# Kernel tuning notes

Measured on AMD Instinct MI355X. Metric: run time of the kernel, lower is better.

## Reference

```python
import jax, jax.numpy as jnp
import numpy as np
import math

C64 = jnp.complex64

def _fftconv_full(a, kern):
    # full linear convolution along last axis (complex), like scipy.signal.fftconvolve
    L = a.shape[-1] + kern.shape[0] - 1
    A = jnp.fft.fft(a, n=L, axis=-1)
    K = jnp.fft.fft(kern.astype(a.dtype), n=L)
    return jnp.fft.ifft(A * K, axis=-1)

def _centered_ifft(f):
    # out[shft] = ifft(f[shft]) * sqrt(N), shft = (arange(N)+fix(N/2)) % N
    N = f.shape[-1]
    shft = (np.arange(N) + int(np.fix(N / 2))) % N
    inv = np.argsort(shft)
    g = jnp.fft.ifft(f[..., shft], axis=-1) * math.sqrt(N)
    return g[..., inv].astype(f.dtype)

def _sincinterp(f):
    # zero-stuff by 2 then sinc-filter; returns length 2N-1 along last axis
    N = f.shape[-1]
    y = jnp.zeros(f.shape[:-1] + (2 * N - 1,), f.dtype).at[..., ::2].set(f)
    kern = jnp.asarray(np.sinc(np.arange(-(2 * N - 3), 2 * N - 2) / 2.0).astype(np.complex64))
    return _fftconv_full(y, kern)[..., 2 * N - 3: 4 * N - 4]

def _frft_chirp(f, a):
    # Ozaktas chirp-convolution discrete FrFT, valid for 0.5 <= a <= 1.5
    N = f.shape[-1]
    alpha = a * math.pi / 2
    tana2, sina = math.tan(alpha / 2), math.sin(alpha)
    fi = _sincinterp(f)                                   # [..., 2N-1]
    pad = jnp.zeros(f.shape[:-1] + (N - 1,), f.dtype)
    fp = jnp.concatenate([pad, fi, pad], axis=-1)         # [..., 4N-3]
    n = np.arange(-2 * N + 2, 2 * N - 1).astype(np.float64)
    chrp = jnp.asarray(np.exp(-1j * math.pi / N * tana2 / 4 * n ** 2).astype(np.complex64))
    fp = chrp * fp
    c = math.pi / N / sina / 4
    m = np.arange(-(4 * N - 4), 4 * N - 3).astype(np.float64)
    kern = jnp.asarray(np.exp(1j * c * m ** 2).astype(np.complex64))
    ret = _fftconv_full(fp, kern)[..., 4 * N - 4: 8 * N - 7] * math.sqrt(c / math.pi)
    ret = chrp * ret
    phase = np.complex64(np.exp(-1j * (1 - a) * math.pi / 4))
    return phase * ret[..., N - 1: 3 * N - 2: 2]          # [..., N]

def _frft_last(f, a):
    # torch branch logic for the a values used here: a=0.5 (fwd), a=-0.5 (inv)
    if a < 0.5:
        f = _centered_ifft(f)
        a = a + 1.0
    return _frft_chirp(f, a)

def _frft2d(x, a):
    t = _frft_last(x, a)                                  # rows: along W
    return jnp.swapaxes(_frft_last(jnp.swapaxes(t, -1, -2), a), -1, -2)  # cols: along H

def _c1x1(x, w, b=None):
    y = jnp.einsum('nchw,oc->nohw', x, w)
    return y if b is None else y + b[None, :, None, None]

def _c3x3(x, w, b):
    y = jax.lax.conv_general_dilated(x, w, (1, 1), 'SAME',
                                     dimension_numbers=('NCHW', 'OIHW', 'NCHW'))
    return y + b[None, :, None, None]

def _forward(x, conv1_w, mag_s_w, mag_s_b, mag_f_w, mag_f_b, mag_w, mag_b,
             pha_w, pha_b, conv_0_w, conv_0_b, conv_1_w, conv_1_b, conv2_w):
    angle = 0.5
    alpha = math.cos(angle * math.pi / 2)
    N, C, H, W = x.shape
    H1, W1 = int(H * alpha), int(W * alpha)
    x1 = _c1x1(x, conv1_w)                                # stride=1 -> downsample is identity
    C1, C0 = C // 4, C // 4 // 3
    x_0, x_05, x_1 = x1[:, :C0], x1[:, C0:C1 - C0], x1[:, C1 - C0:C1]
    h0, w0 = (H - H1) // 2, (W - W1) // 2
    mask1 = jnp.zeros((H, W), jnp.float32).at[h0:h0 + H1, w0:w0 + W1].set(1.0)
    mask2 = 1.0 - mask1
    # fractional Fourier branch
    Fre = _frft2d(x_05.astype(C64), angle)
    mag, pha = jnp.abs(Fre), jnp.angle(Fre)
    mag_out = _c1x1(_c3x3(mag * mask1, mag_s_w, mag_s_b) * mask1
                    + _c1x1(mag * mask2, mag_f_w, mag_f_b) * mask2, mag_w, mag_b)
    pha_out = _c1x1(pha, pha_w, pha_b)
    Fre_out = jax.lax.complex(mag_out * jnp.cos(pha_out), mag_out * jnp.sin(pha_out))
    ifrft = jnp.abs(_frft2d(Fre_out, -angle))
    # plain Fourier branch (conv_1 applied to both mag and pha, as in the source)
    fre = jnp.fft.rfft2(x_1)
    fm, fp = jnp.abs(fre), jnp.angle(fre)
    mo = _c1x1(fm, conv_1_w, conv_1_b)
    po = _c1x1(fp, conv_1_w, conv_1_b)
    x_1o = jnp.fft.irfft2(jax.lax.complex(mo * jnp.cos(po), mo * jnp.sin(po)), s=(H, W))
    x_0o = _c1x1(x_0, conv_0_w, conv_0_b)
    return _c1x1(jnp.concatenate([x_0o, ifrft, x_1o], axis=1), conv2_w)

def setup_inputs():
    key = jax.random.key(0)
    ks = jax.random.split(key, 16)
    N, C, H, W, Co = 4, 192, 128, 128, 192
    C1, C0 = C // 4, C // 4 // 3
    Cm = C1 - 2 * C0
    s = 0.05
    r = lambda k, sh: jax.random.normal(k, sh, jnp.float32)
    return {
        "x": r(ks[0], (N, C, H, W)),
        "conv1_w": r(ks[1], (C1, C)) * s,
        "mag_s_w": r(ks[2], (Cm, Cm, 3, 3)) * s, "mag_s_b": r(ks[3], (Cm,)) * s,
        "mag_f_w": r(ks[4], (Cm, Cm)) * s, "mag_f_b": r(ks[5], (Cm,)) * s,
        "mag_w": r(ks[6], (Cm, Cm)) * s, "mag_b": r(ks[7], (Cm,)) * s,
        "pha_w": r(ks[8], (Cm, Cm)) * s, "pha_b": r(ks[9], (Cm,)) * s,
        "conv_0_w": r(ks[10], (C0, C0)) * s, "conv_0_b": r(ks[11], (C0,)) * s,
        "conv_1_w": r(ks[12], (C0, C0)) * s, "conv_1_b": r(ks[13], (C0,)) * s,
        "conv2_w": r(ks[14], (Co, C1)) * s,
    }

def reference(x, conv1_w, mag_s_w, mag_s_b, mag_f_w, mag_f_b, mag_w, mag_b,
              pha_w, pha_b, conv_0_w, conv_0_b, conv_1_w, conv_1_b, conv2_w):
    return _forward(x, conv1_w, mag_s_w, mag_s_b, mag_f_w, mag_f_b, mag_w, mag_b,
                    pha_w, pha_b, conv_0_w, conv_0_b, conv_1_w, conv_1_b, conv2_w)
```

## Files before the change

### kernel.cpp

```cpp
#include <hip/hip_runtime.h>
#include <math.h>

#define PI_D 3.14159265358979323846
#define TWO_PI_F 6.2831853071795864f

__device__ __align__(16) float2 g_Mf [128*128];
__device__ __align__(16) float2 g_MfT[128*128];
__device__ __align__(16) float2 g_Mb [128*128];
__device__ __align__(16) float2 g_MbT[128*128];
__device__ __align__(16) float2 g_F  [128*128];
__device__ __align__(16) float2 g_IF [128*128];
__device__ __align__(16) float  g_x1 [4*48*16384];
__device__ __align__(16) float2 g_bufA[64*16384];
__device__ __align__(16) float2 g_bufB[64*16384];
__device__ __align__(16) float  g_mag[64*16384];
__device__ __align__(16) float  g_pha[64*16384];
__device__ __align__(16) float  g_m65[64*8320];
__device__ __align__(16) float  g_p65[64*8320];
__device__ __align__(16) float  g_t1 [64*16384];
__device__ __align__(16) float  g_t2 [64*16384];
__device__ __align__(16) float  g_t3 [64*8320];
__device__ __align__(16) float  g_t4 [64*8320];
__device__ __align__(16) float  g_cat[4*48*16384];

__device__ inline void build_A_body(int tid) {
    if (tid >= 128*128) return;
    int o = tid >> 7, m = tid & 127;
    const double chc = -PI_D/128.0 * tan(PI_D/8.0) * 0.25;
    const double c   =  PI_D/(512.0*sin(PI_D/4.0));
    const double inv2pi = 1.0/(2.0*PI_D);
    float sr, si;
    {
        int n1 = 2*m - 127, tt = 2*(o - m);
        double ang = chc*(double)(n1*n1) + c*(double)(tt*tt);
        double r = ang*inv2pi; r -= floor(r);
        float af = (float)(r*2.0*PI_D);
        float sn, cs; __sincosf(af, &sn, &cs);
        sr = cs; si = sn;
    }
    for (int j = 0; j < 127; ++j) {
        int q  = 2*j + 1;
        int n1 = q - 127, tt = 2*o - q, d = q - 2*m;
        double ang = chc*(double)(n1*n1) + c*(double)(tt*tt);
        double r = ang*inv2pi; r -= floor(r);
        float af = (float)(r*2.0*PI_D);
        float s = (((d-1)>>1) & 1) ? -2.0f : 2.0f;
        s /= (3.14159265358979f*(float)d);
        float sn, cs; __sincosf(af, &sn, &cs);
        sr += s*cs; si += s*sn;
    }
    int n2 = 2*o - 127;
    double ph = chc*(double)(n2*n2) - PI_D/8.0;
    double r = ph*inv2pi; r -= floor(r);
    float pf = (float)(r*2.0*PI_D);
    float scale = (float)sqrt(c/PI_D);
    float sn, cs; __sincosf(pf, &sn, &cs);
    float cr = cs*scale, ci = sn*scale;
    float2 v = make_float2(sr*cr - si*ci, sr*ci + si*cr);
    g_Mf[tid] = v;
    g_MfT[(m<<7) + o] = v;
    int p = (o*m) & 127;
    float ang2 = TWO_PI_F*(float)p/128.0f;
    float sn2, cs2; __sincosf(ang2, &sn2, &cs2);
    g_F[tid]  = make_float2(cs2, -sn2);
    g_IF[tid] = make_float2(cs2*0.0078125f, sn2*0.0078125f);
}

template<int LM>
__device__ inline void load_T4(float2* tr, const float* mp, const float* pp,
                               const float* Trl, int hh, int w4) {
    if (LM == 1) {
        float4 v = *(const float4*)(Trl + (hh<<7) + w4);
        tr[0] = make_float2(v.x, 0.f); tr[1] = make_float2(v.y, 0.f);
        tr[2] = make_float2(v.z, 0.f); tr[3] = make_float2(v.w, 0.f);
    } else if (LM == 2) {
#pragma unroll
        for (int i = 0; i < 4; ++i) {
            int idx = (hh<<7) + w4 + i;
            float m = mp[idx], ph = pp[idx];
            float sn, cs; __sincosf(ph, &sn, &cs);
            tr[i] = make_float2(m*cs, m*sn);
        }
    } else {
#pragma unroll
        for (int i = 0; i < 4; ++i) {
            int w = w4 + i;
            int h2 = hh, w2 = w; float sg = 1.f;
            if (w >= 65) { h2 = (128 - hh) & 127; w2 = 128 - w; sg = -1.f; }
            int idx = h2*65 + w2;
            float m = mp[idx], ph = pp[idx];
            float sn, cs; __sincosf(ph, &sn, &cs);
            tr[i] = make_float2(m*cs, sg*m*sn);
        }
    }
}

__device__ inline void cfma(float2& a, float sx, float sy, float mx, float my) {
    a.x = fmaf(sx, mx, a.x); a.x = fmaf(-sy, my, a.x);
    a.y = fmaf(sx, my, a.y); a.y = fmaf(sy, mx, a.y);
}

template<int LM>
__device__ inline void rmul_body(const float2* __restrict__ MT, const float* __restrict__ Trl,
                                 const float* __restrict__ mp_, const float* __restrict__ pp_,
                                 float2* __restrict__ out, int cstart,
                                 int p, int r0, int t, float2* Ssh, float2* Mch) {
    constexpr bool RS = (LM == 1);
    const float* Trp = nullptr; const float* mp = nullptr; const float* pp = nullptr;
    if (LM == 1) { int n = p >> 4, c = p & 15; Trp = Trl + ((long)(n*48 + cstart + c) << 14); }
    if (LM == 2) { mp = mp_ + ((long)p << 14); pp = pp_ + ((long)p << 14); }
    if (LM == 3) { mp = mp_ + (long)p*8320;   pp = pp_ + (long)p*8320; }
    for (int u = t; u < 512; u += 256) {
        int row = u >> 5, w4 = (u & 31) << 2;
        float2 tr4[4];
        load_T4<LM>(tr4, mp, pp, Trp, r0 + row, w4);
        float4* d = (float4*)&Ssh[(row << 7) + w4];
        d[0] = make_float4(tr4[0].x, tr4[0].y, tr4[1].x, tr4[1].y);
        d[1] = make_float4(tr4[2].x, tr4[2].y, tr4[3].x, tr4[3].y);
    }
    float2 acc[4][2] = {};
    int cq = t & 63, rp = t >> 6;
    for (int kc = 0; kc < 128; kc += 16) {
        __syncthreads();
        {
            const float4* Mg = (const float4*)(MT + (kc << 7));
            float4* Md = (float4*)Mch;
            for (int i = t; i < 1024; i += 256) Md[i] = Mg[i];
        }
        __syncthreads();
#pragma unroll
        for (int kk = 0; kk < 16; kk += 2) {
            float4 s2[4];
#pragma unroll
            for (int i = 0; i < 4; ++i)
                s2[i] = *(const float4*)&Ssh[(((rp<<2)+i) << 7) + kc + kk];
            float4 m0 = *(const float4*)&Mch[(kk << 7) + (cq<<1)];
            float4 m1 = *(const float4*)&Mch[((kk+1) << 7) + (cq<<1)];
#pragma unroll
            for (int i = 0; i < 4; ++i) {
                if (RS) {
                    acc[i][0].x = fmaf(s2[i].x, m0.x, acc[i][0].x);
                    acc[i][0].y = fmaf(s2[i].x, m0.y, acc[i][0].y);
                    acc[i][1].x = fmaf(s2[i].x, m0.z, acc[i][1].x);
                    acc[i][1].y = fmaf(s2[i].x, m0.w, acc[i][1].y);
                    acc[i][0].x = fmaf(s2[i].z, m1.x, acc[i][0].x);
                    acc[i][0].y = fmaf(s2[i].z, m1.y, acc[i][0].y);
                    acc[i][1].x = fmaf(s2[i].z, m1.z, acc[i][1].x);
                    acc[i][1].y = fmaf(s2[i].z, m1.w, acc[i][1].y);
                } else {
                    cfma(acc[i][0], s2[i].x, s2[i].y, m0.x, m0.y);
                    cfma(acc[i][1], s2[i].x, s2[i].y, m0.z, m0.w);
                    cfma(acc[i][0], s2[i].z, s2[i].w, m1.x, m1.y);
                    cfma(acc[i][1], s2[i].z, s2[i].w, m1.z, m1.w);
                }
            }
        }
    }
    long base = ((long)p << 14);
#pragma unroll
    for (int i = 0; i < 4; ++i) {
        float4* dst = (float4*)(out + base + ((long)(r0 + (rp<<2) + i) << 7) + (cq<<1));
        *dst = make_float4(acc[i][0].x, acc[i][0].y, acc[i][1].x, acc[i][1].y);
    }
}

template<int EPI>
__device__ inline void lmul_body(const float2* __restrict__ A, const float2* __restrict__ in,
                                 float* __restrict__ o1, float* __restrict__ o2, int coff,
                                 int p, int j0, int t, float2* Ssh, float2* Tch) {
    const float2* T = in + ((long)p << 14);
    {
        const float4* Ag = (const float4*)(A + ((long)j0 << 7));
        float4* Sd = (float4*)Ssh;
        for (int i = t; i < 1024; i += 256) Sd[i] = Ag[i];
    }
    float2 acc[4][2] = {};
    int cq = t & 63, rp = t >> 6;
    for (int kc = 0; kc < 128; kc += 16) {
        __syncthreads();
        {
            const float4* Tg = (const float4*)(T + (kc << 7));
            float4* Td = (float4*)Tch;
            for (int i = t; i < 1024; i += 256) Td[i] = Tg[i];
        }
        __syncthreads();
#pragma unroll
        for (int kk = 0; kk < 16; kk += 2) {
            float4 s2[4];
#pragma unroll
            for (int i = 0; i < 4; ++i)
                s2[i] = *(const float4*)&Ssh[(((rp<<2)+i) << 7) + kc + kk];
            float4 m0 = *(const float4*)&Tch[(kk << 7) + (cq<<1)];
            float4 m1 = *(const float4*)&Tch[((kk+1) << 7) + (cq<<1)];
#pragma unroll
            for (int i = 0; i < 4; ++i) {
                if (EPI == 3) {
                    acc[i][0].x = fmaf(s2[i].x, m0.x, acc[i][0].x);
                    acc[i][0].x = fmaf(-s2[i].y, m0.y, acc[i][0].x);
                    acc[i][1].x = fmaf(s2[i].x, m0.z, acc[i][1].x);
                    acc[i][1].x = fmaf(-s2[i].y, m0.w, acc[i][1].x);
                    acc[i][0].x = fmaf(s2[i].z, m1.x, acc[i][0].x);
                    acc[i][0].x = fmaf(-s2[i].w, m1.y, acc[i][0].x);
                    acc[i][1].x = fmaf(s2[i].z, m1.z, acc[i][1].x);
                    acc[i][1].x = fmaf(-s2[i].w, m1.w, acc[i][1].x);
                } else {
                    cfma(acc[i][0], s2[i].x, s2[i].y, m0.x, m0.y);
                    cfma(acc[i][1], s2[i].x, s2[i].y, m0.z, m0.w);
                    cfma(acc[i][0], s2[i].z, s2[i].w, m1.x, m1.y);
                    cfma(acc[i][1], s2[i].z, s2[i].w, m1.z, m1.w);
                }
            }
        }
    }
#pragma unroll
    for (int i = 0; i < 4; ++i) {
        int jj = j0 + (rp<<2) + i;
        int ww0 = cq << 1;
        float2 v0 = acc[i][0], v1 = acc[i][1];
        if (EPI == 1) {
            long idx = ((long)p << 14) + ((long)jj << 7) + ww0;
            *(float2*)&o1[idx] = make_float2(sqrtf(v0.x*v0.x + v0.y*v0.y),
                                             sqrtf(v1.x*v1.x + v1.y*v1.y));
            *(float2*)&o2[idx] = make_float2(atan2f(v0.y, v0.x), atan2f(v1.y, v1.x));
        } else if (EPI == 2) {
            int n = p >> 4, c = p & 15;
            long idx = ((long)(n*48 + coff + c) << 14) + ((long)jj << 7) + ww0;
            *(float2*)&o1[idx] = make_float2(sqrtf(v0.x*v0.x + v0.y*v0.y),
                                             sqrtf(v1.x*v1.x + v1.y*v1.y));
        } else if (EPI == 3) {
            int n = p >> 4, c = p & 15;
            long idx = ((long)(n*48 + coff + c) << 14) + ((long)jj << 7) + ww0;
            *(float2*)&o1[idx] = make_float2(v0.x, v1.x);
        } else if (EPI == 4) {
            if (ww0 < 65) {
                long idx = (long)p*8320 + jj*65 + ww0;
                o1[idx] = sqrtf(v0.x*v0.x + v0.y*v0.y);
                o2[idx] = atan2f(v0.y, v0.x);
                if (ww0 + 1 < 65) {
                    o1[idx+1] = sqrtf(v1.x*v1.x + v1.y*v1.y);
                    o2[idx+1] = atan2f(v1.y, v1.x);
                }
            }
        }
    }
}

template<int LMA, int LMB>
__global__ __launch_bounds__(256, 4)
void k_rmul_dual(const float2* __restrict__ MTa, const float* __restrict__ TrlA,
                 const float* __restrict__ mpA, const float* __restrict__ ppA,
                 float2* __restrict__ outA, int cstartA,
                 const float2* __restrict__ MTb, const float* __restrict__ TrlB,
                 const float* __restrict__ mpB, const float* __restrict__ ppB,
                 float2* __restrict__ outB, int cstartB) {
    __shared__ float2 Ssh[16*128];
    __shared__ float2 Mch[16*128];
    __shared__ float2 W[128];
    int bx = blockIdx.x, by = blockIdx.y, t = threadIdx.x;
    if (bx >= 128) {
        int b = (bx - 128)*8 + by;
        if (b < 64) {
            if (t < 128) {
                float ang = TWO_PI_F*(float)t/128.0f;
                float sn, cs; __sincosf(ang, &sn, &cs);
                float invs = 0.08838834764831845f;
                W[t] = make_float2(cs*invs, sn*invs);
            }
            __syncthreads();
            int tid = b*256 + t;
            int o = tid >> 7, m = tid & 127;
            float sr = 0.f, si = 0.f;
            for (int r = 0; r < 128; ++r) {
                float2 a = g_Mf[(o<<7) + r];
                int k = ((r+64)*(m+64)) & 127;
                float2 w = W[k];
                sr += a.x*w.x - a.y*w.y;
                si += a.x*w.y + a.y*w.x;
            }
            float2 v = make_float2(sr, si);
            g_Mb[tid] = v;
            g_MbT[(m<<7) + o] = v;
        }
        return;
    }
    int p = bx & 63, r0 = by << 4;
    if (bx < 64) rmul_body<LMA>(MTa, TrlA, mpA, ppA, outA, cstartA, p, r0, t, Ssh, Mch);
    else         rmul_body<LMB>(MTb, TrlB, mpB, ppB, outB, cstartB, p, r0, t, Ssh, Mch);
}

template<int EPIA, int EPIB>
__global__ __launch_bounds__(256, 4)
void k_lmul_dual(const float2* __restrict__ Aa, const float2* __restrict__ inA,
                 float* __restrict__ o1A, float* __restrict__ o2A, int coffA,
                 const float2* __restrict__ Ab, const float2* __restrict__ inB,
                 float* __restrict__ o1B, float* __restrict__ o2B, int coffB) {
    __shared__ float2 Ssh[16*128];
    __shared__ float2 Tch[16*128];
    int bx = blockIdx.x, j0 = blockIdx.y << 4, t = threadIdx.x;
    int p = bx & 63;
    if (bx < 64) lmul_body<EPIA>(Aa, inA, o1A, o2A, coffA, p, j0, t, Ssh, Tch);
    else         lmul_body<EPIB>(Ab, inB, o1B, o2B, coffB, p, j0, t, Ssh, Tch);
}

template<int CIN, int COUT, int KSPLIT, int OSPLIT>
__device__ inline void wconv_body(const float* __restrict__ in, const float* __restrict__ wgt,
                                  const float* __restrict__ bias, float* __restrict__ out,
                                  int S, int Ctin, int cstart, int Ctout, int costart,
                                  int n, int sblk, float* red) {
    constexpr int OW = COUT / OSPLIT;
    constexpr int KC = CIN / KSPLIT;
    int t = threadIdx.x, lane = t & 63;
    int wv = __builtin_amdgcn_readfirstlane(t >> 6);
    int oq = wv / KSPLIT, kq = wv % KSPLIT;
    int s0 = sblk << 7;
    const float* inb = in + ((long)(n*Ctin + cstart + kq*KC))*S + s0 + (lane<<1);
    const float* wb  = wgt + (oq*OW)*CIN + kq*KC;
    float2 acc[OW];
#pragma unroll
    for (int j = 0; j < OW; ++j) acc[j] = make_float2(0.f, 0.f);
#pragma unroll 4
    for (int c = 0; c < KC; ++c) {
        float2 xv = *(const float2*)(inb + (long)c*S);
#pragma unroll
        for (int j = 0; j < OW; ++j) {
            float w = wb[j*CIN + c];
            acc[j].x = fmaf(w, xv.x, acc[j].x);
            acc[j].y = fmaf(w, xv.y, acc[j].y);
        }
    }
    if (KSPLIT == 1) {
#pragma unroll
        for (int j = 0; j < OW; ++j) {
            int o = oq*OW + j;
            float b = bias ? bias[o] : 0.f;
            *(float2*)(out + ((long)(n*Ctout + costart + o))*S + s0 + (lane<<1))
                = make_float2(acc[j].x + b, acc[j].y + b);
        }
    } else {
#pragma unroll
        for (int j = 0; j < OW; ++j) {
            int o = oq*OW + j;
            *(float2*)&red[((kq*COUT + o) << 7) + (lane<<1)] = acc[j];
        }
        __syncthreads();
        for (int idx = t; idx < COUT*64; idx += 256) {
            int o = idx >> 6, l2 = (idx & 63) << 1;
            float b = bias ? bias[o] : 0.f;
            float2 v = make_float2(b, b);
#pragma unroll
            for (int k2 = 0; k2 < KSPLIT; ++k2) {
                float2 r = *(const float2*)&red[((k2*COUT + o) << 7) + l2];
                v.x += r.x; v.y += r.y;
            }
            *(float2*)(out + ((long)(n*Ctout + costart + o))*S + s0 + l2) = v;
        }
    }
}

__global__ __launch_bounds__(256, 1)
void k_conv1_build(const float* __restrict__ x, const float* __restrict__ w,
                   float* __restrict__ x1) {
    __shared__ float red[2*48*128];
    if (blockIdx.z == 0) {
        wconv_body<192,48,2,2>(x, w, nullptr, x1, 16384, 192, 0, 48, 0,
                               blockIdx.y, blockIdx.x, red);
    } else {
        int b = blockIdx.y*gridDim.x + blockIdx.x;
        if (b < 64) build_A_body(b*256 + threadIdx.x);
    }
}

__global__ __launch_bounds__(256, 1)
void k_conv2(const float* __restrict__ in, const float* __restrict__ wgt,
             float* __restrict__ out) {
    __shared__ float red[1];
    wconv_body<48,192,1,4>(in, wgt, nullptr, out, 16384, 48, 0, 192, 0,
                           blockIdx.y, blockIdx.x, red);
}

__device__ inline void mix16b(const float* __restrict__ in, const float* __restrict__ w,
                              const float* __restrict__ b, float* __restrict__ out,
                              int Ctin, int S, int n, int s0) {
    int t = threadIdx.x, lane = t & 63;
    int oq = __builtin_amdgcn_readfirstlane(t >> 6);
    const float* inb = in + ((long)(n*Ctin))*S + s0 + (lane<<1);
    float2 xv[16];
#pragma unroll
    for (int c = 0; c < 16; ++c) xv[c] = *(const float2*)(inb + (long)c*S);
#pragma unroll
    for (int j = 0; j < 4; ++j) {
        int o = oq*4 + j;
        float bb = b ? b[o] : 0.f;
        float2 a = make_float2(bb, bb);
#pragma unroll
        for (int c = 0; c < 16; ++c) {
            float ww = w[o*16 + c];
            a.x = fmaf(ww, xv[c].x, a.x);
            a.y = fmaf(ww, xv[c].y, a.y);
        }
        *(float2*)(out + ((long)(n*Ctin + o))*S + s0 + (lane<<1)) = a;
    }
}

__device__ inline void maskconv_body(const float* __restrict__ mag, const float* __restrict__ ws3,
                                     const float* __restrict__ bs, const float* __restrict__ wf,
                                     const float* __restrict__ bf, const float* __restrict__ wm,
                                     const float* __restrict__ bm, float* __restrict__ out,
                                     int n, int tile, float (*patch)[324]) {
    int h0 = (tile >> 3) << 4, w0 = (tile & 7) << 4;
    int t = threadIdx.x;
    const float* magn = mag + ((long)n << 18);
    for (int idx = t; idx < 16*324; idx += 256) {
        int c = idx / 324, r = idx - c*324;
        int ph = r / 18, pw = r - ph*18;
        int gh = h0 - 1 + ph, gw = w0 - 1 + pw;
        float v = 0.f;
        if (gh >= 19 && gh < 109 && gw >= 19 && gw < 109)
            v = magn[(c<<14) + (gh<<7) + gw];
        patch[c][r] = v;
    }
    __syncthreads();
    int ty = t >> 4, tx = t & 15;
    int h = h0 + ty, w = w0 + tx;
    bool in1 = (h >= 19 && h < 109 && w >= 19 && w < 109);
    unsigned long long bal = __ballot(in1);
    float res[16];
    if (bal != 0ull) {
        float acc[16];
#pragma unroll
        for (int o = 0; o < 16; ++o) acc[o] = bs[o];
        for (int c = 0; c < 16; ++c) {
            float tap[9];
#pragma unroll
            for (int dh = 0; dh < 3; ++dh)
#pragma unroll
                for (int dw = 0; dw < 3; ++dw)
                    tap[dh*3+dw] = patch[c][(ty+dh)*18 + tx+dw];
            const float* wp = ws3 + c*9;
#pragma unroll
            for (int o = 0; o < 16; ++o)
#pragma unroll
                for (int k = 0; k < 9; ++k)
                    acc[o] = fmaf(wp[o*144 + k], tap[k], acc[o]);
        }
#pragma unroll
        for (int o = 0; o < 16; ++o) res[o] = acc[o];
    }
    if (bal != ~0ull) {
        float xv[16];
#pragma unroll
        for (int c = 0; c < 16; ++c) xv[c] = magn[(c<<14) + (h<<7) + w];
#pragma unroll
        for (int o = 0; o < 16; ++o) {
            float a = bf[o];
#pragma unroll
            for (int c = 0; c < 16; ++c) a = fmaf(wf[o*16 + c], xv[c], a);
            if (!in1) res[o] = a;
        }
    }
#pragma unroll
    for (int o2 = 0; o2 < 16; ++o2) {
        float a = bm[o2];
#pragma unroll
        for (int o = 0; o < 16; ++o)
            a = fmaf(wm[o2*16 + o], res[o], a);
        out[((long)((n<<4) + o2) << 14) + (h << 7) + w] = a;
    }
}

__global__ __launch_bounds__(256, 2)
void k_point(const float* __restrict__ mag, const float* __restrict__ ws3,
             const float* __restrict__ bs, const float* __restrict__ wf,
             const float* __restrict__ bf, const float* __restrict__ wm,
             const float* __restrict__ bm, float* __restrict__ t2,
             const float* __restrict__ pha, const float* __restrict__ pw,
             const float* __restrict__ pb, float* __restrict__ t1,
             const float* __restrict__ x1, const float* __restrict__ c0w,
             const float* __restrict__ c0b, float* __restrict__ cat,
             const float* __restrict__ m65, const float* __restrict__ p65,
             const float* __restrict__ c1w, const float* __restrict__ c1b,
             float* __restrict__ t3, float* __restrict__ t4) {
    __shared__ float patch[16][324];
    int b = blockIdx.x;
    if (b < 256) {
        maskconv_body(mag, ws3, bs, wf, bf, wm, bm, t2, b >> 6, b & 63, patch);
    } else if (b < 768) {
        int i = b - 256;
        mix16b(pha, pw, pb, t1, 16, 16384, i >> 7, (i & 127) << 7);
    } else if (b < 1280) {
        int i = b - 768;
        mix16b(x1, c0w, c0b, cat, 48, 16384, i >> 7, (i & 127) << 7);
    } else if (b < 1540) {
        int i = b - 1280;
        mix16b(m65, c1w, c1b, t3, 16, 8320, i / 65, (i % 65) << 7);
    } else {
        int i = b - 1540;
        mix16b(p65, c1w, c1b, t4, 16, 8320, i / 65, (i % 65) << 7);
    }
}

extern "C" void kernel_launch(void* const* d_in, const int* in_sizes, int n_in,
                              void* d_out, int out_size, void* d_ws, size_t ws_size,
                              hipStream_t stream) {
    (void)in_sizes; (void)n_in; (void)out_size; (void)d_ws; (void)ws_size;
    const float* x        = (const float*)d_in[0];
    const float* conv1_w  = (const float*)d_in[1];
    const float* mag_s_w  = (const float*)d_in[2];
    const float* mag_s_b  = (const float*)d_in[3];
    const float* mag_f_w  = (const float*)d_in[4];
    const float* mag_f_b  = (const float*)d_in[5];
    const float* mag_w_   = (const float*)d_in[6];
    const float* mag_b_   = (const float*)d_in[7];
    const float* pha_w_   = (const float*)d_in[8];
    const float* pha_b_   = (const float*)d_in[9];
    const float* conv_0_w = (const float*)d_in[10];
    const float* conv_0_b = (const float*)d_in[11];
    const float* conv_1_w = (const float*)d_in[12];
    const float* conv_1_b = (const float*)d_in[13];
    const float* conv2_w  = (const float*)d_in[14];
    float* outp = (float*)d_out;

    float2 *Mf, *MfT, *Mb, *MbT, *Fm, *IFm, *bufA, *bufB;
    float *x1, *mag, *pha, *m65, *p65, *t1, *t2, *t3, *t4, *cat;
    hipGetSymbolAddress((void**)&Mf,   HIP_SYMBOL(g_Mf));
    hipGetSymbolAddress((void**)&MfT,  HIP_SYMBOL(g_MfT));
    hipGetSymbolAddress((void**)&Mb,   HIP_SYMBOL(g_Mb));
    hipGetSymbolAddress((void**)&MbT,  HIP_SYMBOL(g_MbT));
    hipGetSymbolAddress((void**)&Fm,   HIP_SYMBOL(g_F));
    hipGetSymbolAddress((void**)&IFm,  HIP_SYMBOL(g_IF));
    hipGetSymbolAddress((void**)&bufA, HIP_SYMBOL(g_bufA));
    hipGetSymbolAddress((void**)&bufB, HIP_SYMBOL(g_bufB));
    hipGetSymbolAddress((void**)&x1,   HIP_SYMBOL(g_x1));
    hipGetSymbolAddress((void**)&mag,  HIP_SYMBOL(g_mag));
    hipGetSymbolAddress((void**)&pha,  HIP_SYMBOL(g_pha));
    hipGetSymbolAddress((void**)&m65,  HIP_SYMBOL(g_m65));
    hipGetSymbolAddress((void**)&p65,  HIP_SYMBOL(g_p65));
    hipGetSymbolAddress((void**)&t1,   HIP_SYMBOL(g_t1));
    hipGetSymbolAddress((void**)&t2,   HIP_SYMBOL(g_t2));
    hipGetSymbolAddress((void**)&t3,   HIP_SYMBOL(g_t3));
    hipGetSymbolAddress((void**)&t4,   HIP_SYMBOL(g_t4));
    hipGetSymbolAddress((void**)&cat,  HIP_SYMBOL(g_cat));

    dim3 bt(256, 1, 1);

    k_conv1_build<<<dim3(128,4,2), bt, 0, stream>>>(x, conv1_w, x1);

    k_rmul_dual<1,1><<<dim3(136,8), bt, 0, stream>>>(
        MfT, x1, nullptr, nullptr, bufA, 16,
        Fm,  x1, nullptr, nullptr, bufB, 32);

    k_lmul_dual<1,4><<<dim3(128,8), bt, 0, stream>>>(
        Mf, bufA, mag, pha, 0,
        Fm, bufB, m65, p65, 0);

    k_point<<<1800, bt, 0, stream>>>(mag, mag_s_w, mag_s_b, mag_f_w, mag_f_b,
                                     mag_w_, mag_b_, t2,
                                     pha, pha_w_, pha_b_, t1,
                                     x1, conv_0_w, conv_0_b, cat,
                                     m65, p65, conv_1_w, conv_1_b, t3, t4);

    k_rmul_dual<2,3><<<dim3(128,8), bt, 0, stream>>>(
        MbT, nullptr, t2, t1, bufA, 0,
        IFm, nullptr, t3, t4, bufB, 0);

    k_lmul_dual<2,3><<<dim3(128,8), bt, 0, stream>>>(
        Mb,  bufA, cat, nullptr, 16,
        IFm, bufB, cat, nullptr, 32);

    k_conv2<<<dim3(128,4), bt, 0, stream>>>(cat, conv2_w, outp);
}
```

Before: 328.7 us.

## Split k_point output channels across 4 waves with 1024-thread blocks

Reorganises the fused pointwise/mask-conv kernel to use 1024-thread blocks. Each group of 256 threads computes 4 of the 16 output channels instead of one thread computing all 16. The 3x3 mask-conv stage now exchanges its intermediate results through shared memory before the final 16x16 mix. The mix16b blocks cover 4 pixel groups per block with an early-exit bound. The aim is lower register pressure and more wave parallelism per pixel, at the cost of extra syncs and LDS traffic, and the interior-pixel path now runs only 4 output channels per thread.

```diff
diff --git a/kernel.cpp b/kernel.cpp
--- a/kernel.cpp
+++ b/kernel.cpp
@@ -380,25 +380,39 @@
 
 __device__ inline void mix16b(const float* __restrict__ in, const float* __restrict__ w,
                               const float* __restrict__ b, float* __restrict__ out,
-                              int Ctin, int S, int n, int s0) {
+                              int Ctin, int S, int n, int s0base, int Slim) {
     int t = threadIdx.x, lane = t & 63;
-    int oq = __builtin_amdgcn_readfirstlane(t >> 6);
+    int wv = __builtin_amdgcn_readfirstlane(t >> 6);
+    int oq = wv & 3, pg = wv >> 2;
+    int s0 = s0base + (pg << 7);
+    if (s0 >= Slim) return;
     const float* inb = in + ((long)(n*Ctin))*S + s0 + (lane<<1);
-    float2 xv[16];
-#pragma unroll
-    for (int c = 0; c < 16; ++c) xv[c] = *(const float2*)(inb + (long)c*S);
+    float2 acc[4];
+#pragma unroll
+    for (int j = 0; j < 4; ++j) {
+        float bb = b ? b[oq*4 + j] : 0.f;
+        acc[j] = make_float2(bb, bb);
+    }
+#pragma unroll
+    for (int half = 0; half < 2; ++half) {
+        float2 xv[8];
+#pragma unroll
+        for (int c = 0; c < 8; ++c)
+            xv[c] = *(const float2*)(inb + (long)(half*8 + c)*S);
+#pragma unroll
+        for (int c = 0; c < 8; ++c) {
+#pragma unroll
+            for (int j = 0; j < 4; ++j) {
+                float ww = w[(oq*4 + j)*16 + half*8 + c];
+                acc[j].x = fmaf(ww, xv[c].x, acc[j].x);
+                acc[j].y = fmaf(ww, xv[c].y, acc[j].y);
+            }
+        }
+    }
 #pragma unroll
     for (int j = 0; j < 4; ++j) {
         int o = oq*4 + j;
-        float bb = b ? b[o] : 0.f;
-        float2 a = make_float2(bb, bb);
-#pragma unroll
-        for (int c = 0; c < 16; ++c) {
-            float ww = w[o*16 + c];
-            a.x = fmaf(ww, xv[c].x, a.x);
-            a.y = fmaf(ww, xv[c].y, a.y);
-        }
-        *(float2*)(out + ((long)(n*Ctin + o))*S + s0 + (lane<<1)) = a;
+        *(float2*)(out + ((long)(n*Ctin + o))*S + s0 + (lane<<1)) = acc[j];
     }
 }
 
@@ -406,69 +420,88 @@
                                      const float* __restrict__ bs, const float* __restrict__ wf,
                                      const float* __restrict__ bf, const float* __restrict__ wm,
                                      const float* __restrict__ bm, float* __restrict__ out,
-                                     int n, int tile, float (*patch)[324]) {
+                                     int n, int tile, float* patch) {
     int h0 = (tile >> 3) << 4, w0 = (tile & 7) << 4;
     int t = threadIdx.x;
     const float* magn = mag + ((long)n << 18);
-    for (int idx = t; idx < 16*324; idx += 256) {
+    for (int idx = t; idx < 16*324; idx += 1024) {
         int c = idx / 324, r = idx - c*324;
         int ph = r / 18, pw = r - ph*18;
         int gh = h0 - 1 + ph, gw = w0 - 1 + pw;
         float v = 0.f;
         if (gh >= 19 && gh < 109 && gw >= 19 && gw < 109)
             v = magn[(c<<14) + (gh<<7) + gw];
-        patch[c][r] = v;
+        patch[c*324 + r] = v;
     }
     __syncthreads();
-    int ty = t >> 4, tx = t & 15;
+    int oq = t >> 8, pix = t & 255;
+    int ty = pix >> 4, tx = pix & 15;
     int h = h0 + ty, w = w0 + tx;
     bool in1 = (h >= 19 && h < 109 && w >= 19 && w < 109);
     unsigned long long bal = __ballot(in1);
-    float res[16];
+    float res[4];
     if (bal != 0ull) {
-        float acc[16];
-#pragma unroll
-        for (int o = 0; o < 16; ++o) acc[o] = bs[o];
+        float acc[4];
+#pragma unroll
+        for (int j = 0; j < 4; ++j) acc[j] = bs[oq*4 + j];
         for (int c = 0; c < 16; ++c) {
-            float tap[9];
-#pragma unroll
-            for (int dh = 0; dh < 3; ++dh)
-#pragma unroll
-                for (int dw = 0; dw < 3; ++dw)
-                    tap[dh*3+dw] = patch[c][(ty+dh)*18 + tx+dw];
-            const float* wp = ws3 + c*9;
-#pragma unroll
-            for (int o = 0; o < 16; ++o)
-#pragma unroll
-                for (int k = 0; k < 9; ++k)
-                    acc[o] = fmaf(wp[o*144 + k], tap[k], acc[o]);
-        }
-#pragma unroll
-        for (int o = 0; o < 16; ++o) res[o] = acc[o];
+            const float* pc = patch + c*324 + ty*18 + tx;
+            const float* wc = ws3 + c*9;
+#pragma unroll
+            for (int dh = 0; dh < 3; ++dh) {
+#pragma unroll
+                for (int dw = 0; dw < 3; ++dw) {
+                    float tap = pc[dh*18 + dw];
+#pragma unroll
+                    for (int j = 0; j < 4; ++j)
+                        acc[j] = fmaf(wc[(oq*4 + j)*144 + dh*3 + dw], tap, acc[j]);
+                }
+            }
+        }
+#pragma unroll
+        for (int j = 0; j < 4; ++j) res[j] = acc[j];
     }
     if (bal != ~0ull) {
-        float xv[16];
-#pragma unroll
-        for (int c = 0; c < 16; ++c) xv[c] = magn[(c<<14) + (h<<7) + w];
-#pragma unroll
-        for (int o = 0; o < 16; ++o) {
-            float a = bf[o];
-#pragma unroll
-            for (int c = 0; c < 16; ++c) a = fmaf(wf[o*16 + c], xv[c], a);
-            if (!in1) res[o] = a;
-        }
-    }
-#pragma unroll
-    for (int o2 = 0; o2 < 16; ++o2) {
+        float acc2[4];
+#pragma unroll
+        for (int j = 0; j < 4; ++j) acc2[j] = bf[oq*4 + j];
+#pragma unroll
+        for (int half = 0; half < 2; ++half) {
+            float xv[8];
+#pragma unroll
+            for (int c = 0; c < 8; ++c)
+                xv[c] = magn[((half*8 + c)<<14) + (h<<7) + w];
+#pragma unroll
+            for (int c = 0; c < 8; ++c)
+#pragma unroll
+                for (int j = 0; j < 4; ++j)
+                    acc2[j] = fmaf(wf[(oq*4 + j)*16 + half*8 + c], xv[c], acc2[j]);
+        }
+        if (!in1) {
+#pragma unroll
+            for (int j = 0; j < 4; ++j) res[j] = acc2[j];
+        }
+    }
+    __syncthreads();
+    float* resl = patch;
+#pragma unroll
+    for (int j = 0; j < 4; ++j) resl[(oq*4 + j)*256 + pix] = res[j];
+    __syncthreads();
+    float rr[16];
+#pragma unroll
+    for (int o = 0; o < 16; ++o) rr[o] = resl[o*256 + pix];
+#pragma unroll
+    for (int j = 0; j < 4; ++j) {
+        int o2 = oq*4 + j;
         float a = bm[o2];
 #pragma unroll
         for (int o = 0; o < 16; ++o)
-            a = fmaf(wm[o2*16 + o], res[o], a);
+            a = fmaf(wm[o2*16 + o], rr[o], a);
         out[((long)((n<<4) + o2) << 14) + (h << 7) + w] = a;
     }
 }
 
-__global__ __launch_bounds__(256, 2)
+__global__ __launch_bounds__(1024, 8)
 void k_point(const float* __restrict__ mag, const float* __restrict__ ws3,
              const float* __restrict__ bs, const float* __restrict__ wf,
              const float* __restrict__ bf, const float* __restrict__ wm,
@@ -480,22 +513,22 @@
              const float* __restrict__ m65, const float* __restrict__ p65,
              const float* __restrict__ c1w, const float* __restrict__ c1b,
              float* __restrict__ t3, float* __restrict__ t4) {
-    __shared__ float patch[16][324];
+    __shared__ float patch[16*324];
     int b = blockIdx.x;
     if (b < 256) {
         maskconv_body(mag, ws3, bs, wf, bf, wm, bm, t2, b >> 6, b & 63, patch);
-    } else if (b < 768) {
+    } else if (b < 384) {
         int i = b - 256;
-        mix16b(pha, pw, pb, t1, 16, 16384, i >> 7, (i & 127) << 7);
-    } else if (b < 1280) {
-        int i = b - 768;
-        mix16b(x1, c0w, c0b, cat, 48, 16384, i >> 7, (i & 127) << 7);
-    } else if (b < 1540) {
-        int i = b - 1280;
-        mix16b(m65, c1w, c1b, t3, 16, 8320, i / 65, (i % 65) << 7);
+        mix16b(pha, pw, pb, t1, 16, 16384, i >> 5, (i & 31) << 9, 16384);
+    } else if (b < 512) {
+        int i = b - 384;
+        mix16b(x1, c0w, c0b, cat, 48, 16384, i >> 5, (i & 31) << 9, 16384);
+    } else if (b < 580) {
+        int i = b - 512;
+        mix16b(m65, c1w, c1b, t3, 16, 8320, i / 17, (i % 17) << 9, 8320);
     } else {
-        int i = b - 1540;
-        mix16b(p65, c1w, c1b, t4, 16, 8320, i / 65, (i % 65) << 7);
+        int i = b - 580;
+        mix16b(p65, c1w, c1b, t4, 16, 8320, i / 17, (i % 17) << 9, 8320);
     }
 }
 
@@ -553,11 +586,11 @@
         Mf, bufA, mag, pha, 0,
         Fm, bufB, m65, p65, 0);
 
-    k_point<<<1800, bt, 0, stream>>>(mag, mag_s_w, mag_s_b, mag_f_w, mag_f_b,
-                                     mag_w_, mag_b_, t2,
-                                     pha, pha_w_, pha_b_, t1,
-                                     x1, conv_0_w, conv_0_b, cat,
-                                     m65, p65, conv_1_w, conv_1_b, t3, t4);
+    k_point<<<648, dim3(1024,1,1), 0, stream>>>(mag, mag_s_w, mag_s_b, mag_f_w, mag_f_b,
+                                                mag_w_, mag_b_, t2,
+                                                pha, pha_w_, pha_b_, t1,
+                                                x1, conv_0_w, conv_0_b, cat,
+                                                m65, p65, conv_1_w, conv_1_b, t3, t4);
 
     k_rmul_dual<2,3><<<dim3(128,8), bt, 0, stream>>>(
         MbT, nullptr, t2, t1, bufA, 0,
```

Measured after the change: 326.3 us. Within noise of the previous version (-0.7%).
